# Kernel optimization log

Hardware: AMD Instinct MI355X
Metric: run time of the kernel (lower is better)

Reference implementation:

```python
import jax, jax.numpy as jnp
import numpy as np

B, L, D = 2, 2048, 1024
H, K = 16, 16
HD = D // H


def setup_inputs() -> dict:
    key = jax.random.key(0)
    k1, k2, k3, k4, k5 = jax.random.split(key, 5)
    x = jax.random.normal(k1, (B, L, D), dtype=jnp.float32)
    # Linear weight (out_features, in_features), small init to keep logits sane
    w_in = jax.random.normal(k2, (3 * D, D), dtype=jnp.float32) * 0.02
    # TISA radial-basis kernel parameters, per (head, kernel)
    kernel_offsets = jax.random.normal(k3, (H, K), dtype=jnp.float32) * 20.0
    kernel_amplitudes = 0.1 + 0.01 * jax.random.normal(k4, (H, K), dtype=jnp.float32)
    kernel_sharpness = 0.1 + 0.01 * jax.random.normal(k5, (H, K), dtype=jnp.float32)
    return {"x": x, "w_in": w_in, "kernel_offsets": kernel_offsets,
            "kernel_amplitudes": kernel_amplitudes, "kernel_sharpness": kernel_sharpness}


def tisa_bias(offsets, amplitudes, sharpness, seq_len):
    # relative positions -(L-1) .. (L-1)  -> per-head RBF positional scores
    rel = jnp.arange(-(seq_len - 1), seq_len, dtype=jnp.float32)  # (2L-1,)
    # scores[h, m] = sum_k amp[h,k] * exp(-|sharp[h,k]| * (off[h,k] - rel[m])^2)
    diff = offsets[:, :, None] - rel[None, None, :]               # (H, K, 2L-1)
    scores = jnp.sum(amplitudes[:, :, None] * jnp.exp(-jnp.abs(sharpness)[:, :, None] * diff * diff), axis=1)  # (H, 2L-1)
    # Toeplitz expansion: bias[h, i, j] = scores[h, (i - j) + (L-1)]
    i = jnp.arange(seq_len)
    idx = i[:, None] - i[None, :] + (seq_len - 1)                 # (L, L)
    return scores[:, idx]                                         # (H, L, L)


def reference(x, w_in, kernel_offsets, kernel_amplitudes, kernel_sharpness):
    b, l, d = x.shape
    proj = jnp.einsum('bld,ed->ble', x, w_in)                     # (B, L, 3D)
    # split: memory = first 2D (k then v), query = last D
    k_, v_, q_ = proj[..., :d], proj[..., d:2 * d], proj[..., 2 * d:]

    def heads(t):
        return t.reshape(b, l, H, HD).transpose(0, 2, 1, 3)       # (B, H, L, HD)

    q, k, v = heads(q_), heads(k_), heads(v_)
    bias = tisa_bias(kernel_offsets, kernel_amplitudes, kernel_sharpness, l)  # (H, L, L)
    scale = 1.0 / np.sqrt(HD).astype(np.float32)
    logits = jnp.einsum('bhld,bhmd->bhlm', q, k) * scale + bias[None]
    attn = jax.nn.softmax(logits, axis=-1)
    out = jnp.einsum('bhlm,bhmd->bhld', attn, v)                  # (B, H, L, HD)
    return out.transpose(0, 2, 1, 3).reshape(b, l, d)             # (B, L, D)
```

## Files before the change

### kernel.cpp

```cpp
#include <hip/hip_runtime.h>
#include <hip/hip_bf16.h>
#include <stdint.h>
#include <stddef.h>


#define NB     2
#define NH     16
#define SL     2048
#define DH     64
#define DMODEL 1024
#define SCP    4096
#define LOG2E  1.44269504088896340736f

typedef __attribute__((ext_vector_type(8)))  short bf16x8;
typedef __attribute__((ext_vector_type(4)))  short bf16x4;
typedef __attribute__((ext_vector_type(4)))  float f32x4;
typedef __attribute__((ext_vector_type(16))) float f32x16;

static __device__ __forceinline__ short f2bf(float x) {
  __hip_bfloat16 h = __float2bfloat16(x);
  return *reinterpret_cast<short*>(&h);
}
static __device__ __forceinline__ short f2bf_fast(float x) {
  union { float f; uint32_t u; } v; v.f = x;
  return (short)((v.u + 0x8000u) >> 16);
}
static __device__ __forceinline__ long long bf4_to_ll(bf16x4 v) {
  long long r; __builtin_memcpy(&r, &v, 8); return r;
}
static __device__ __forceinline__ bf16x4 ll_to_bf4(long long v) {
  bf16x4 r; __builtin_memcpy(&r, &v, 8); return r;
}
static __device__ __forceinline__ float fexp2(float x) {
#if __has_builtin(__builtin_amdgcn_exp2f)
  return __builtin_amdgcn_exp2f(x);
#else
  return __expf(x * 0.69314718056f);
#endif
}
#define GLD(g, l) __builtin_amdgcn_global_load_lds( \
    (const __attribute__((address_space(1))) void*)(g), \
    (__attribute__((address_space(3))) void*)(l), 16, 0, 0)

__global__ __launch_bounds__(256) void prep_k(
    const float* __restrict__ x, const float* __restrict__ w,
    const float* __restrict__ koff, const float* __restrict__ kamp,
    const float* __restrict__ kshp,
    short* __restrict__ xbf, short* __restrict__ wbf,
    float* __restrict__ scores) {
  const int bx = blockIdx.x, tid = threadIdx.x;
  if (bx < 7168) {
    const float* src = (bx < 4096) ? x : w;
    short* dst       = (bx < 4096) ? xbf : wbf;
    const int i      = (bx < 4096 ? bx : bx - 4096) * 256 + tid;
    float4 a = *(const float4*)(src + (size_t)i * 4);
    bf16x4 o;
    o.x = f2bf(a.x); o.y = f2bf(a.y); o.z = f2bf(a.z); o.w = f2bf(a.w);
    *(bf16x4*)(dst + (size_t)i * 4) = o;
  } else {
    const int idx = bx - 7168;
    const int h = idx >> 4;
    const int r = (idx & 15) * 256 + tid;
    if (r >= 4095) return;
    float rel = (float)(r - (SL - 1));
    float acc = 0.f;
#pragma unroll
    for (int k = 0; k < 16; ++k) {
      float o = koff[h * 16 + k];
      float a = kamp[h * 16 + k];
      float s = fabsf(kshp[h * 16 + k]);
      float d = o - rel;
      acc += a * __expf(-s * d * d);
    }
    scores[h * SCP + r] = acc * LOG2E;
  }
}

__global__ __launch_bounds__(256) void qkv_gemm_k(
    const short* __restrict__ A, const short* __restrict__ Bw,
    __hip_bfloat16* __restrict__ kbuf, __hip_bfloat16* __restrict__ vbufT,
    __hip_bfloat16* __restrict__ qbuf) {
  __shared__ __align__(16) short SM[12288];
  short* As = SM;
  short* Bs = SM + 8192;
  const int tid  = threadIdx.x;
  const int lane = tid & 63;
  const int wv   = tid >> 6;
  const int l15  = lane & 15, quad = lane >> 4;
  const int wm = (wv & 1) * 64, wn = (wv >> 1) * 32;
  const int xt = blockIdx.x, yt = blockIdx.y;
  const int m0 = yt * 128, n0 = xt * 64;
  const int which = xt >> 4;
  const int hh    = xt & 15;

  f32x4 acc[4][2];
#pragma unroll
  for (int r = 0; r < 4; ++r)
#pragma unroll
    for (int c = 0; c < 2; ++c) acc[r][c] = (f32x4){0.f, 0.f, 0.f, 0.f};

  for (int kt = 0; kt < 16; ++kt) {
    const int k0 = kt * 64;
#pragma unroll
    for (int it = 0; it < 4; ++it) {
      const int e8  = it * 256 + tid;
      GLD(A + (size_t)(m0 + (e8 >> 3)) * DMODEL + k0 + (e8 & 7) * 8, &As[e8 * 8]);
    }
#pragma unroll
    for (int it = 0; it < 2; ++it) {
      const int e8  = it * 256 + tid;
      GLD(Bw + (size_t)(n0 + (e8 >> 3)) * DMODEL + k0 + (e8 & 7) * 8, &Bs[e8 * 8]);
    }
    __syncthreads();
#pragma unroll
    for (int ki = 0; ki < 64; ki += 32) {
      bf16x8 af[4], bfv[2];
#pragma unroll
      for (int r = 0; r < 4; ++r)
        af[r] = *(const bf16x8*)&As[(wm + r * 16 + l15) * 64 + ki + quad * 8];
#pragma unroll
      for (int c = 0; c < 2; ++c)
        bfv[c] = *(const bf16x8*)&Bs[(wn + c * 16 + l15) * 64 + ki + quad * 8];
#pragma unroll
      for (int r = 0; r < 4; ++r)
#pragma unroll
        for (int c = 0; c < 2; ++c)
          acc[r][c] = __builtin_amdgcn_mfma_f32_16x16x32_bf16(af[r], bfv[c], acc[r][c], 0, 0, 0);
    }
    __syncthreads();
  }

  const int bb  = m0 >> 11;
  const int llb = m0 & 2047;
  if (which != 1) {
    const float qs = (which == 2) ? 0.125f * LOG2E : 1.0f;
#pragma unroll
    for (int r = 0; r < 4; ++r)
#pragma unroll
      for (int c = 0; c < 2; ++c)
#pragma unroll
        for (int gg = 0; gg < 4; ++gg)
          SM[(wm + r * 16 + quad * 4 + gg) * 72 + wn + c * 16 + l15] =
              f2bf_fast(acc[r][c][gg] * qs);
    __syncthreads();
    __hip_bfloat16* dst = (which == 0) ? kbuf : qbuf;
#pragma unroll
    for (int i = 0; i < 4; ++i) {
      const int cidx = i * 256 + tid;
      const int m = cidx >> 3, ch = cidx & 7;
      bf16x8 val = *(const bf16x8*)&SM[m * 72 + ch * 8];
      *(bf16x8*)&dst[(((size_t)bb * NH + hh) * SL + llb + m) * DH + ch * 8] = val;
    }
  } else {
#pragma unroll
    for (int r = 0; r < 4; ++r)
#pragma unroll
      for (int c = 0; c < 2; ++c) {
        bf16x4 pk;
#pragma unroll
        for (int gg = 0; gg < 4; ++gg) pk[gg] = f2bf_fast(acc[r][c][gg]);
        *(bf16x4*)&SM[(wn + c * 16 + l15) * 136 + wm + r * 16 + quad * 4] = pk;
      }
    __syncthreads();
#pragma unroll
    for (int i = 0; i < 4; ++i) {
      const int cidx = i * 256 + tid;
      const int n = cidx >> 4, ch = cidx & 15;
      bf16x8 val = *(const bf16x8*)&SM[n * 136 + ch * 8];
      *(bf16x8*)&vbufT[(((size_t)bb * NH + hh) * DH + n) * SL + llb + ch * 8] = val;
    }
  }
}

__global__ __launch_bounds__(128, 2) void attn_k(
    const __hip_bfloat16* __restrict__ qbuf, const __hip_bfloat16* __restrict__ kbuf,
    const __hip_bfloat16* __restrict__ vbufT, const float* __restrict__ scores,
    float* __restrict__ out) {
  __shared__ __align__(16) short Ks[2][64 * 72];
  __shared__ __align__(16) short Vs[2][64 * 72];
  __shared__ __align__(16) float Bt[2][128];
  const int bh   = blockIdx.x;
  const int b    = bh >> 4, h = bh & 15;
  const int tid  = threadIdx.x;
  const int lane = tid & 63;
  const int wv   = tid >> 6;
  const int n32  = lane & 31, hf = lane >> 5;
  const int i0b  = blockIdx.y * 64;
  const int i0   = i0b + wv * 32;
  const __hip_bfloat16* qb = qbuf + (size_t)bh * SL * DH;
  const short* kb = (const short*)(kbuf + (size_t)bh * SL * DH);
  const short* vb = (const short*)(vbufT + (size_t)bh * DH * SL);
  const float* sc = scores + h * SCP;

  bf16x8 qf[4];
#pragma unroll
  for (int kc = 0; kc < 4; ++kc)
    qf[kc] = *(const bf16x8*)&qb[(size_t)(i0 + n32) * DH + kc * 16 + hf * 8];

  f32x16 ot[2];
#pragma unroll
  for (int dt = 0; dt < 2; ++dt)
#pragma unroll
    for (int r = 0; r < 16; ++r) ot[dt][r] = 0.f;
  float lsum = 0.f;

  auto stage = [&](int bsel, int j0) {
    const short* ksrc = kb + (size_t)j0 * DH;
#pragma unroll
    for (int i = 0; i < 4; ++i) {
      int c = i * 128 + tid; int r = c / 9, s = c - r * 9;
      GLD(ksrc + (size_t)r * DH + s * 8, &Ks[bsel][c * 8]);
    }
    if (tid < 64) {
      int c = 512 + tid; int r = c / 9, s = c - r * 9;
      GLD(ksrc + (size_t)r * DH + s * 8, &Ks[bsel][c * 8]);
    }
#pragma unroll
    for (int i = 0; i < 4; ++i) {
      int c = i * 128 + tid; int r = c / 9, s = c - r * 9;
      GLD(vb + (size_t)r * SL + j0 + s * 8, &Vs[bsel][c * 8]);
    }
    if (tid < 64) {
      int c = 512 + tid; int r = c / 9, s = c - r * 9;
      GLD(vb + (size_t)r * SL + j0 + s * 8, &Vs[bsel][c * 8]);
    }
    if (tid < 32) GLD(sc + (i0b - j0 + 1984) + tid * 4, &Bt[bsel][tid * 4]);
  };

  auto compute = [&](int bsel) {
    const short* Kp = Ks[bsel];
    const short* Vp = Vs[bsel];
    const float* Bp = Bt[bsel];
#pragma unroll
    for (int kt = 0; kt < 2; ++kt) {
      f32x16 st;
#pragma unroll
      for (int r = 0; r < 16; ++r) st[r] = 0.f;
      __builtin_amdgcn_s_setprio(1);
#pragma unroll
      for (int kc = 0; kc < 4; ++kc) {
        bf16x8 kf = *(const bf16x8*)&Kp[(kt * 32 + n32) * 72 + kc * 16 + hf * 8];
        st = __builtin_amdgcn_mfma_f32_32x32x16_bf16(kf, qf[kc], st, 0, 0, 0);
      }
      __builtin_amdgcn_s_setprio(0);
      bf16x4 pk[4];
      const int tb0 = wv * 32 + n32 - kt * 32 - 4 * hf + 63;
#pragma unroll
      for (int g = 0; g < 4; ++g) {
        const int tb = tb0 - 8 * g;
#pragma unroll
        for (int i = 0; i < 4; ++i) {
          const float p = fexp2(st[g * 4 + i] + Bp[tb - i]);
          lsum += p;
          pk[g][i] = f2bf_fast(p);
        }
      }
      long long s0 = hf ? bf4_to_ll(pk[0]) : bf4_to_ll(pk[1]);
      bf16x4 r0 = ll_to_bf4(__shfl_xor(s0, 32));
      bf16x8 pf0 = hf == 0 ? __builtin_shufflevector(pk[0], r0, 0, 1, 2, 3, 4, 5, 6, 7)
                           : __builtin_shufflevector(r0, pk[1], 0, 1, 2, 3, 4, 5, 6, 7);
      long long s1 = hf ? bf4_to_ll(pk[2]) : bf4_to_ll(pk[3]);
      bf16x4 r1 = ll_to_bf4(__shfl_xor(s1, 32));
      bf16x8 pf1 = hf == 0 ? __builtin_shufflevector(pk[2], r1, 0, 1, 2, 3, 4, 5, 6, 7)
                           : __builtin_shufflevector(r1, pk[3], 0, 1, 2, 3, 4, 5, 6, 7);
      __builtin_amdgcn_s_setprio(1);
#pragma unroll
      for (int dt = 0; dt < 2; ++dt) {
        const short* vr = &Vp[(dt * 32 + n32) * 72 + kt * 32];
        bf16x8 vf0 = *(const bf16x8*)&vr[hf * 8];
        bf16x8 vf1 = *(const bf16x8*)&vr[16 + hf * 8];
        ot[dt] = __builtin_amdgcn_mfma_f32_32x32x16_bf16(vf0, pf0, ot[dt], 0, 0, 0);
        ot[dt] = __builtin_amdgcn_mfma_f32_32x32x16_bf16(vf1, pf1, ot[dt], 0, 0, 0);
      }
      __builtin_amdgcn_s_setprio(0);
    }
  };

  stage(0, 0);
  __syncthreads();
  int cur = 0;
  for (int j0 = 64; j0 < SL; j0 += 64) {
    stage(cur ^ 1, j0);
    compute(cur);
    __syncthreads();
    cur ^= 1;
  }
  compute(cur);

  lsum += __shfl_xor(lsum, 32);
  const float inv = 1.f / lsum;
  float* orow = out + (((size_t)b * SL + i0 + n32) * NH + h) * DH;
#pragma unroll
  for (int dt = 0; dt < 2; ++dt)
#pragma unroll
    for (int g = 0; g < 4; ++g) {
      f32x4 v;
#pragma unroll
      for (int i = 0; i < 4; ++i) v[i] = ot[dt][g * 4 + i] * inv;
      *(f32x4*)&orow[dt * 32 + 8 * g + 4 * hf] = v;
    }
}

extern "C" void kernel_launch(void* const* d_in, const int* in_sizes, int n_in,
                              void* d_out, int out_size, void* d_ws, size_t ws_size,
                              hipStream_t stream) {
  const float* x    = (const float*)d_in[0];
  const float* w    = (const float*)d_in[1];
  const float* koff = (const float*)d_in[2];
  const float* kamp = (const float*)d_in[3];
  const float* kshp = (const float*)d_in[4];
  float* out = (float*)d_out;

  const size_t per = (size_t)NB * NH * SL * DH;
  const size_t nx  = (size_t)NB * SL * DMODEL;
  const size_t nw  = (size_t)3 * DMODEL * DMODEL;

  __hip_bfloat16* kbuf  = (__hip_bfloat16*)d_ws;
  __hip_bfloat16* vbufT = kbuf + per;
  __hip_bfloat16* qbuf  = vbufT + per;
  float* scores = (float*)(qbuf + per);
  short* xbf    = (short*)(scores + (size_t)NH * SCP);
  short* wbf    = xbf + nx;

  prep_k<<<7424, 256, 0, stream>>>(x, w, koff, kamp, kshp, xbf, wbf, scores);
  qkv_gemm_k<<<dim3(48, 32), 256, 0, stream>>>(xbf, wbf, kbuf, vbufT, qbuf);
  attn_k<<<dim3(NB * NH, SL / 64), 128, 0, stream>>>(qbuf, kbuf, vbufT, scores, out);
}
```

Baseline: 187.1 us.

## Split attention KV tile across wave pairs with LDS reduction of partial outputs

The attention kernel now runs 256 threads per block. Each pair of waves covers the same 32 query rows but takes a different 32-key half of each 64-key tile, and the two partial outputs and row sums are combined through LDS at the end. The positional bias is preloaded into the MFMA accumulator, so a separate add is no longer needed, and row sums are spread over four accumulators. This doubles waves per block to improve latency hiding and shortens each wave's serial chain per tile, at the cost of an extra barrier and LDS reduction plus duplicated Q fragment loads.

```diff
diff --git a/kernel.cpp b/kernel.cpp
--- a/kernel.cpp
+++ b/kernel.cpp
@@ -172,7 +172,7 @@
   }
 }
 
-__global__ __launch_bounds__(128, 2) void attn_k(
+__global__ __launch_bounds__(256, 4) void attn_k(
     const __hip_bfloat16* __restrict__ qbuf, const __hip_bfloat16* __restrict__ kbuf,
     const __hip_bfloat16* __restrict__ vbufT, const float* __restrict__ scores,
     float* __restrict__ out) {
@@ -183,7 +183,9 @@
   const int b    = bh >> 4, h = bh & 15;
   const int tid  = threadIdx.x;
   const int lane = tid & 63;
-  const int wv   = tid >> 6;
+  const int w    = tid >> 6;
+  const int wv   = w & 1;
+  const int kw   = w >> 1;
   const int n32  = lane & 31, hf = lane >> 5;
   const int i0b  = blockIdx.y * 64;
   const int i0   = i0b + wv * 32;
@@ -202,13 +204,13 @@
   for (int dt = 0; dt < 2; ++dt)
 #pragma unroll
     for (int r = 0; r < 16; ++r) ot[dt][r] = 0.f;
-  float lsum = 0.f;
+  float ls[4] = {0.f, 0.f, 0.f, 0.f};
 
   auto stage = [&](int bsel, int j0) {
     const short* ksrc = kb + (size_t)j0 * DH;
 #pragma unroll
-    for (int i = 0; i < 4; ++i) {
-      int c = i * 128 + tid; int r = c / 9, s = c - r * 9;
+    for (int i = 0; i < 2; ++i) {
+      int c = i * 256 + tid; int r = c / 9, s = c - r * 9;
       GLD(ksrc + (size_t)r * DH + s * 8, &Ks[bsel][c * 8]);
     }
     if (tid < 64) {
@@ -216,8 +218,8 @@
       GLD(ksrc + (size_t)r * DH + s * 8, &Ks[bsel][c * 8]);
     }
 #pragma unroll
-    for (int i = 0; i < 4; ++i) {
-      int c = i * 128 + tid; int r = c / 9, s = c - r * 9;
+    for (int i = 0; i < 2; ++i) {
+      int c = i * 256 + tid; int r = c / 9, s = c - r * 9;
       GLD(vb + (size_t)r * SL + j0 + s * 8, &Vs[bsel][c * 8]);
     }
     if (tid < 64) {
@@ -231,49 +233,46 @@
     const short* Kp = Ks[bsel];
     const short* Vp = Vs[bsel];
     const float* Bp = Bt[bsel];
-#pragma unroll
-    for (int kt = 0; kt < 2; ++kt) {
-      f32x16 st;
-#pragma unroll
-      for (int r = 0; r < 16; ++r) st[r] = 0.f;
-      __builtin_amdgcn_s_setprio(1);
-#pragma unroll
-      for (int kc = 0; kc < 4; ++kc) {
-        bf16x8 kf = *(const bf16x8*)&Kp[(kt * 32 + n32) * 72 + kc * 16 + hf * 8];
-        st = __builtin_amdgcn_mfma_f32_32x32x16_bf16(kf, qf[kc], st, 0, 0, 0);
-      }
-      __builtin_amdgcn_s_setprio(0);
-      bf16x4 pk[4];
-      const int tb0 = wv * 32 + n32 - kt * 32 - 4 * hf + 63;
-#pragma unroll
-      for (int g = 0; g < 4; ++g) {
-        const int tb = tb0 - 8 * g;
-#pragma unroll
-        for (int i = 0; i < 4; ++i) {
-          const float p = fexp2(st[g * 4 + i] + Bp[tb - i]);
-          lsum += p;
-          pk[g][i] = f2bf_fast(p);
-        }
-      }
-      long long s0 = hf ? bf4_to_ll(pk[0]) : bf4_to_ll(pk[1]);
-      bf16x4 r0 = ll_to_bf4(__shfl_xor(s0, 32));
-      bf16x8 pf0 = hf == 0 ? __builtin_shufflevector(pk[0], r0, 0, 1, 2, 3, 4, 5, 6, 7)
-                           : __builtin_shufflevector(r0, pk[1], 0, 1, 2, 3, 4, 5, 6, 7);
-      long long s1 = hf ? bf4_to_ll(pk[2]) : bf4_to_ll(pk[3]);
-      bf16x4 r1 = ll_to_bf4(__shfl_xor(s1, 32));
-      bf16x8 pf1 = hf == 0 ? __builtin_shufflevector(pk[2], r1, 0, 1, 2, 3, 4, 5, 6, 7)
-                           : __builtin_shufflevector(r1, pk[3], 0, 1, 2, 3, 4, 5, 6, 7);
-      __builtin_amdgcn_s_setprio(1);
-#pragma unroll
-      for (int dt = 0; dt < 2; ++dt) {
-        const short* vr = &Vp[(dt * 32 + n32) * 72 + kt * 32];
-        bf16x8 vf0 = *(const bf16x8*)&vr[hf * 8];
-        bf16x8 vf1 = *(const bf16x8*)&vr[16 + hf * 8];
-        ot[dt] = __builtin_amdgcn_mfma_f32_32x32x16_bf16(vf0, pf0, ot[dt], 0, 0, 0);
-        ot[dt] = __builtin_amdgcn_mfma_f32_32x32x16_bf16(vf1, pf1, ot[dt], 0, 0, 0);
-      }
-      __builtin_amdgcn_s_setprio(0);
-    }
+    f32x16 st;
+    const int tb0 = wv * 32 + n32 - kw * 32 - 4 * hf + 63;
+#pragma unroll
+    for (int g = 0; g < 4; ++g)
+#pragma unroll
+      for (int i = 0; i < 4; ++i) st[g * 4 + i] = Bp[tb0 - 8 * g - i];
+    __builtin_amdgcn_s_setprio(1);
+#pragma unroll
+    for (int kc = 0; kc < 4; ++kc) {
+      bf16x8 kf = *(const bf16x8*)&Kp[(kw * 32 + n32) * 72 + kc * 16 + hf * 8];
+      st = __builtin_amdgcn_mfma_f32_32x32x16_bf16(kf, qf[kc], st, 0, 0, 0);
+    }
+    __builtin_amdgcn_s_setprio(0);
+    bf16x4 pk[4];
+#pragma unroll
+    for (int g = 0; g < 4; ++g)
+#pragma unroll
+      for (int i = 0; i < 4; ++i) {
+        const float p = fexp2(st[g * 4 + i]);
+        ls[g] += p;
+        pk[g][i] = f2bf_fast(p);
+      }
+    long long s0 = hf ? bf4_to_ll(pk[0]) : bf4_to_ll(pk[1]);
+    bf16x4 r0 = ll_to_bf4(__shfl_xor(s0, 32));
+    bf16x8 pf0 = hf == 0 ? __builtin_shufflevector(pk[0], r0, 0, 1, 2, 3, 4, 5, 6, 7)
+                         : __builtin_shufflevector(r0, pk[1], 0, 1, 2, 3, 4, 5, 6, 7);
+    long long s1 = hf ? bf4_to_ll(pk[2]) : bf4_to_ll(pk[3]);
+    bf16x4 r1 = ll_to_bf4(__shfl_xor(s1, 32));
+    bf16x8 pf1 = hf == 0 ? __builtin_shufflevector(pk[2], r1, 0, 1, 2, 3, 4, 5, 6, 7)
+                         : __builtin_shufflevector(r1, pk[3], 0, 1, 2, 3, 4, 5, 6, 7);
+    __builtin_amdgcn_s_setprio(1);
+#pragma unroll
+    for (int dt = 0; dt < 2; ++dt) {
+      const short* vr = &Vp[(dt * 32 + n32) * 72 + kw * 32];
+      bf16x8 vf0 = *(const bf16x8*)&vr[hf * 8];
+      bf16x8 vf1 = *(const bf16x8*)&vr[16 + hf * 8];
+      ot[dt] = __builtin_amdgcn_mfma_f32_32x32x16_bf16(vf0, pf0, ot[dt], 0, 0, 0);
+      ot[dt] = __builtin_amdgcn_mfma_f32_32x32x16_bf16(vf1, pf1, ot[dt], 0, 0, 0);
+    }
+    __builtin_amdgcn_s_setprio(0);
   };
 
   stage(0, 0);
@@ -286,19 +285,47 @@
     cur ^= 1;
   }
   compute(cur);
-
+  __syncthreads();
+
+  float lsum = (ls[0] + ls[1]) + (ls[2] + ls[3]);
   lsum += __shfl_xor(lsum, 32);
-  const float inv = 1.f / lsum;
-  float* orow = out + (((size_t)b * SL + i0 + n32) * NH + h) * DH;
-#pragma unroll
-  for (int dt = 0; dt < 2; ++dt)
-#pragma unroll
-    for (int g = 0; g < 4; ++g) {
-      f32x4 v;
-#pragma unroll
-      for (int i = 0; i < 4; ++i) v[i] = ot[dt][g * 4 + i] * inv;
-      *(f32x4*)&orow[dt * 32 + 8 * g + 4 * hf] = v;
-    }
+  float* red = (float*)&Ks[0][0];
+  const int rbase = (wv * 64 + lane) * 36;
+  if (kw == 1) {
+#pragma unroll
+    for (int dt = 0; dt < 2; ++dt)
+#pragma unroll
+      for (int g = 0; g < 4; ++g) {
+        f32x4 v;
+#pragma unroll
+        for (int i = 0; i < 4; ++i) v[i] = ot[dt][g * 4 + i];
+        *(f32x4*)&red[rbase + dt * 16 + g * 4] = v;
+      }
+    red[rbase + 32] = lsum;
+  }
+  __syncthreads();
+  if (kw == 0) {
+#pragma unroll
+    for (int dt = 0; dt < 2; ++dt)
+#pragma unroll
+      for (int g = 0; g < 4; ++g) {
+        f32x4 v = *(const f32x4*)&red[rbase + dt * 16 + g * 4];
+#pragma unroll
+        for (int i = 0; i < 4; ++i) ot[dt][g * 4 + i] += v[i];
+      }
+    lsum += red[rbase + 32];
+    const float inv = 1.f / lsum;
+    float* orow = out + (((size_t)b * SL + i0 + n32) * NH + h) * DH;
+#pragma unroll
+    for (int dt = 0; dt < 2; ++dt)
+#pragma unroll
+      for (int g = 0; g < 4; ++g) {
+        f32x4 v;
+#pragma unroll
+        for (int i = 0; i < 4; ++i) v[i] = ot[dt][g * 4 + i] * inv;
+        *(f32x4*)&orow[dt * 32 + 8 * g + 4 * hf] = v;
+      }
+  }
 }
 
 extern "C" void kernel_launch(void* const* d_in, const int* in_sizes, int n_in,
@@ -324,5 +351,5 @@
 
   prep_k<<<7424, 256, 0, stream>>>(x, w, koff, kamp, kshp, xbf, wbf, scores);
   qkv_gemm_k<<<dim3(48, 32), 256, 0, stream>>>(xbf, wbf, kbuf, vbufT, qbuf);
-  attn_k<<<dim3(NB * NH, SL / 64), 128, 0, stream>>>(qbuf, kbuf, vbufT, scores, out);
-}
+  attn_k<<<dim3(NB * NH, SL / 64), 256, 0, stream>>>(qbuf, kbuf, vbufT, scores, out);
+}
```

Result: faster. 179.5 us (-4.1%).
